# Kernel optimization log

Measured on AMD Instinct MI355X. Metric: run time of the kernel, lower is better.

The kernel has to match this reference:

```python
import jax, jax.numpy as jnp
import numpy as np
from jax import lax
import math

B, L, DQ, DK, DV = 4, 1024, 256, 256, 256
H, DE, DOUT, MAX_POS = 8, 64, 512, 32


def conv1d(x, w, b):
    # x: [b, c_in, l], w: [c_out, c_in, 3], pad=1 stride=1
    y = lax.conv_general_dilated(x, w, (1,), [(1, 1)],
                                 dimension_numbers=('NCH', 'OIH', 'NCH'))
    return y + b[None, :, None]


def aij(w_pos, n, max_pos):
    # relative-position table gather -> [q, k, d]
    idx = jnp.arange(n)
    rel = jnp.clip(idx[None, :] - idx[:, None], -max_pos, max_pos) + max_pos
    return w_pos[rel]


def setup_inputs() -> dict:
    key = jax.random.key(0)
    ks = jax.random.split(key, 12)
    s = 0.05
    return {
        'q': jax.random.normal(ks[0], (B, L, DQ), jnp.float32),
        'k': jax.random.normal(ks[1], (B, L, DK), jnp.float32),
        'v': jax.random.normal(ks[2], (B, L, DV), jnp.float32),
        'Wq': jax.random.normal(ks[3], (H * DE, DQ, 3), jnp.float32) * s,
        'bq': jnp.zeros((H * DE,), jnp.float32),
        'Wk': jax.random.normal(ks[4], (H * DE, DK, 3), jnp.float32) * s,
        'bk': jnp.zeros((H * DE,), jnp.float32),
        'Wv': jax.random.normal(ks[5], (DOUT, DV, 3), jnp.float32) * s,
        'bv': jnp.zeros((DOUT,), jnp.float32),
        'Wfc': jax.random.normal(ks[6], (DOUT, DOUT), jnp.float32) * s,
        'bfc': jnp.zeros((DOUT,), jnp.float32),
        'w_pos': jax.random.normal(ks[7], (2 * MAX_POS + 1, DE), jnp.float32),
        'attn_mask': jax.random.randint(ks[8], (1, 1, L, L), 0, 2) > 0,
        'valid_mask': jnp.zeros((1,), jnp.float32),
    }


def reference(q, k, v, Wq, bq, Wk, bk, Wv, bv, Wfc, bfc, w_pos, attn_mask, valid_mask):
    b, n_k = k.shape[0], k.shape[1]
    # b l c -> b c l, conv projections
    Q = conv1d(jnp.swapaxes(q, 1, 2), Wq, bq)   # [b, H*DE, l]
    K = conv1d(jnp.swapaxes(k, 1, 2), Wk, bk)
    V = conv1d(jnp.swapaxes(v, 1, 2), Wv, bv)   # [b, DOUT, l]
    # b (h d) l -> b h l d
    def split_heads(x, h):
        bb, hd, l = x.shape
        return jnp.transpose(x.reshape(bb, h, hd // h, l), (0, 1, 3, 2))
    Q_ = split_heads(Q, H)
    K_ = split_heads(K, H)
    V_ = split_heads(V, H)
    A = jnp.einsum('bhqd,bhkd->bhqk', Q_, K_) / math.sqrt(DE)
    A = A + jnp.einsum('bhqd,qkd->bhqk', Q_, aij(w_pos, n_k, MAX_POS))
    A = jnp.where(attn_mask, -jnp.inf, A)
    A = jax.nn.softmax(A, axis=-1)
    A = A * (A > valid_mask).astype(A.dtype)
    O = jnp.einsum('bhqk,bhkd->bhqd', A, V_)
    # b h n d -> b n (h d)
    O = jnp.transpose(O, (0, 2, 1, 3)).reshape(b, -1, DOUT)
    out = O @ Wfc.T + bfc
    return out, A
```

## Files before the change

### kernel.cpp

```cpp
#include <hip/hip_runtime.h>
#include <math.h>

typedef _Float16 f16;
typedef _Float16 f16x4 __attribute__((ext_vector_type(4)));
typedef _Float16 f16x8 __attribute__((ext_vector_type(8)));
typedef float f32x4 __attribute__((ext_vector_type(4)));

constexpr int B    = 4;
constexpr int L    = 1024;
constexpr int CIN  = 256;
constexpr int H    = 8;
constexpr int DOUT = 512;

__global__ void pack_kernel(const float* __restrict__ Wq, const float* __restrict__ Wk,
                            const float* __restrict__ Wv, f16* __restrict__ Wp)
{
    const int proj = blockIdx.y;
    const int co   = blockIdx.x;
    const int ci   = threadIdx.x;
    const float* W = (proj == 0) ? Wq : (proj == 1) ? Wk : Wv;
    f16* dst = Wp + ((size_t)proj * 512 + co) * 768;
    const float* src = W + (size_t)co * 768 + ci * 3;
    dst[0 * 256 + ci] = (f16)src[0];
    dst[1 * 256 + ci] = (f16)src[1];
    dst[2 * 256 + ci] = (f16)src[2];
}

__global__ __launch_bounds__(256) void convg_kernel(
    const float* __restrict__ qx, const float* __restrict__ kx, const float* __restrict__ vx,
    const f16* __restrict__ Wp,
    const float* __restrict__ bq, const float* __restrict__ bk, const float* __restrict__ bv,
    f16* __restrict__ Qh, f16* __restrict__ Kh, f16* __restrict__ Vt)
{
    const int proj = blockIdx.z;
    const float* __restrict__ x    = (proj == 0) ? qx : (proj == 1) ? kx : vx;
    const float* __restrict__ bias = (proj == 0) ? bq : (proj == 1) ? bk : bv;

    const int mt = blockIdx.x;
    const int b  = mt >> 3;
    const int l0 = (mt & 7) * 128;
    const int nb = blockIdx.y * 128;
    const int tid  = threadIdx.x;
    const int wvid = tid >> 6;
    const int lane = tid & 63;
    const int lg16 = lane & 15;
    const int lg4  = lane >> 4;
    const int wr = wvid >> 1, wc = wvid & 1;

    __shared__ __align__(16) f16 smem[3 * 128 * 72];
    f16* const Ah = smem;
    f16* const Al = smem + 128 * 72;
    f16* const Bs = smem + 2 * 128 * 72;
    f16* const Ct = smem;

    f32x4 acc[4][4];
#pragma unroll
    for (int mi = 0; mi < 4; ++mi)
#pragma unroll
        for (int ni = 0; ni < 4; ++ni) acc[mi][ni] = (f32x4){0.f, 0.f, 0.f, 0.f};

    const int r_st = tid >> 1;
    const int c_st = (tid & 1) * 32;

    for (int kc = 0; kc < 12; ++kc) {
        const int t = kc >> 2, ci0 = (kc & 3) << 6;
        __syncthreads();
        {
            const int l = l0 + r_st + t - 1;
            const bool ok = (l >= 0) && (l < L);
            const float* sx = x + ((size_t)b * L + (ok ? l : 0)) * CIN + ci0 + c_st;
#pragma unroll
            for (int g = 0; g < 4; ++g) {
                float4 v0 = make_float4(0.f, 0.f, 0.f, 0.f), v1 = v0;
                if (ok) { v0 = ((const float4*)sx)[g * 2]; v1 = ((const float4*)sx)[g * 2 + 1]; }
                float vv[8] = {v0.x, v0.y, v0.z, v0.w, v1.x, v1.y, v1.z, v1.w};
                f16 h8[8], l8[8];
#pragma unroll
                for (int i = 0; i < 8; ++i) {
                    h8[i] = (f16)vv[i];
                    l8[i] = (f16)(vv[i] - (float)h8[i]);
                }
                *(float4*)&Ah[r_st * 72 + c_st + g * 8] = *(const float4*)h8;
                *(float4*)&Al[r_st * 72 + c_st + g * 8] = *(const float4*)l8;
            }
        }
        {
            const f16* sw = Wp + ((size_t)proj * 512 + nb + r_st) * 768 + kc * 64 + c_st;
#pragma unroll
            for (int g = 0; g < 4; ++g)
                *(float4*)&Bs[r_st * 72 + c_st + g * 8] = ((const float4*)sw)[g];
        }
        __syncthreads();

#pragma unroll
        for (int ks = 0; ks < 2; ++ks) {
            f16x8 bb[4];
#pragma unroll
            for (int ni = 0; ni < 4; ++ni)
                bb[ni] = *(const f16x8*)&Bs[(wc * 64 + ni * 16 + lg16) * 72 + ks * 32 + lg4 * 8];
#pragma unroll
            for (int mi = 0; mi < 4; ++mi) {
                const f16x8 ah = *(const f16x8*)&Ah[(wr * 64 + mi * 16 + lg16) * 72 + ks * 32 + lg4 * 8];
                const f16x8 al = *(const f16x8*)&Al[(wr * 64 + mi * 16 + lg16) * 72 + ks * 32 + lg4 * 8];
#pragma unroll
                for (int ni = 0; ni < 4; ++ni) {
                    acc[mi][ni] = __builtin_amdgcn_mfma_f32_16x16x32_f16(ah, bb[ni], acc[mi][ni], 0, 0, 0);
                    acc[mi][ni] = __builtin_amdgcn_mfma_f32_16x16x32_f16(al, bb[ni], acc[mi][ni], 0, 0, 0);
                }
            }
        }
    }

    float bvv[4];
#pragma unroll
    for (int ni = 0; ni < 4; ++ni) bvv[ni] = bias[nb + wc * 64 + ni * 16 + lg16];
    __syncthreads();

    if (proj < 2) {
#pragma unroll
        for (int mi = 0; mi < 4; ++mi)
#pragma unroll
            for (int ni = 0; ni < 4; ++ni)
#pragma unroll
                for (int jr = 0; jr < 4; ++jr)
                    Ct[(wr * 64 + mi * 16 + lg4 * 4 + jr) * 136 + wc * 64 + ni * 16 + lg16] =
                        (f16)(acc[mi][ni][jr] + bvv[ni]);
        __syncthreads();
        f16* __restrict__ outp = (proj == 0) ? Qh : Kh;
        const int r = tid >> 1, hh = tid & 1;
        const int bh = b * 8 + (nb >> 6) + hh;
        float4* dst = (float4*)&outp[((size_t)bh * L + l0 + r) * 64];
        const float4* srcp = (const float4*)&Ct[r * 136 + hh * 64];
#pragma unroll
        for (int i = 0; i < 8; ++i) dst[i] = srcp[i];
    } else {
#pragma unroll
        for (int mi = 0; mi < 4; ++mi)
#pragma unroll
            for (int ni = 0; ni < 4; ++ni) {
                f16x4 pk = {(f16)(acc[mi][ni][0] + bvv[ni]), (f16)(acc[mi][ni][1] + bvv[ni]),
                            (f16)(acc[mi][ni][2] + bvv[ni]), (f16)(acc[mi][ni][3] + bvv[ni])};
                *(f16x4*)&Ct[(wc * 64 + ni * 16 + lg16) * 136 + wr * 64 + mi * 16 + lg4 * 4] = pk;
            }
        __syncthreads();
        const int r = tid >> 1, hh = tid & 1;
        float4* dst = (float4*)&Vt[((size_t)b * 512 + nb + r) * L + l0 + hh * 64];
        const float4* srcp = (const float4*)&Ct[r * 136 + hh * 64];
#pragma unroll
        for (int i = 0; i < 8; ++i) dst[i] = srcp[i];
    }
}

__global__ __launch_bounds__(256) void attn_kernel(
    const f16* __restrict__ Qh, const f16* __restrict__ Kh, const f16* __restrict__ Vt,
    const float* __restrict__ w_pos, const int* __restrict__ amask,
    const float* __restrict__ vmaskp,
    float* __restrict__ Aout, f16* __restrict__ Oh)
{
    const int bh = blockIdx.y;
    const int b = bh >> 3, h = bh & 7;
    const int q0 = blockIdx.x * 64;
    const int tid = threadIdx.x;
    const int wv   = tid >> 6;
    const int lane = tid & 63;
    const int lg16 = lane & 15;
    const int lg4  = lane >> 4;

    __shared__ __align__(16) f16  smem_h[4608 * 4];
    __shared__ __align__(16) float Ps[64 * 66];
    f16* const Qs = smem_h;
    f16* const Ks = smem_h + 4608;
    f16* const Vs = smem_h + 2 * 4608;
    f16* const es = smem_h + 3 * 4608;
    f16* const wps = Ks;

    float4 kreg[2], vreg[2];
#pragma unroll
    for (int p = 0; p < 2; ++p) {
        const int it = tid + p * 256, row = it >> 3, ch = it & 7;
        kreg[p] = *(const float4*)&Kh[((size_t)bh * L + row) * 64 + ch * 8];
        vreg[p] = *(const float4*)&Vt[((size_t)(bh * 64 + row)) * L + ch * 8];
    }

    for (int i = tid; i < 512; i += 256) {
        const int row = i >> 3, ch = i & 7;
        *(float4*)&Qs[row * 72 + ch * 8] =
            *(const float4*)&Qh[((size_t)bh * L + q0 + row) * 64 + ch * 8];
    }
    for (int i = tid; i < 640; i += 256) {
        const int r = i >> 3, ch = i & 7;
        f16 t[8];
        if (r < 65) {
            const float* s = w_pos + (size_t)r * 64 + ch * 8;
#pragma unroll
            for (int j = 0; j < 8; ++j) t[j] = (f16)s[j];
        } else {
#pragma unroll
            for (int j = 0; j < 8; ++j) t[j] = (f16)0.f;
        }
        *(float4*)&wps[r * 72 + ch * 8] = *(const float4*)t;
    }
    __syncthreads();

    f16x8 qa[2];
#pragma unroll
    for (int kc = 0; kc < 2; ++kc)
        qa[kc] = *(const f16x8*)&Qs[(wv * 16 + lg16) * 72 + kc * 32 + lg4 * 8];

#pragma unroll
    for (int c = 0; c < 5; ++c) {
        f32x4 acc = {0.f, 0.f, 0.f, 0.f};
#pragma unroll
        for (int kc = 0; kc < 2; ++kc) {
            f16x8 wb = *(const f16x8*)&wps[(c * 16 + lg16) * 72 + kc * 32 + lg4 * 8];
            acc = __builtin_amdgcn_mfma_f32_16x16x32_f16(qa[kc], wb, acc, 0, 0, 0);
        }
        const int r = c * 16 + lg16;
        if (r < 65) {
#pragma unroll
            for (int j = 0; j < 4; ++j)
                Ps[(wv * 16 + lg4 * 4 + j) * 66 + r] = acc[j];
        }
    }

    float mrow[4], lrow[4];
#pragma unroll
    for (int j = 0; j < 4; ++j) { mrow[j] = -INFINITY; lrow[j] = 0.f; }
    f32x4 Oc[4];
#pragma unroll
    for (int c = 0; c < 4; ++c) Oc[c] = (f32x4){0.f, 0.f, 0.f, 0.f};

    const int qloc0 = wv * 16 + lg4 * 4;
    const size_t Abase = ((size_t)bh * L + q0 + qloc0) * L;

    for (int kt = 0; kt < 16; ++kt) {
        const int kbase = kt * 64;
        __syncthreads();
#pragma unroll
        for (int p = 0; p < 2; ++p) {
            const int it = tid + p * 256, row = it >> 3, ch = it & 7;
            *(float4*)&Ks[row * 72 + ch * 8] = kreg[p];
            *(float4*)&Vs[row * 72 + ch * 8] = vreg[p];
        }
        __syncthreads();
        if (kt < 15) {
            const int kb2 = kbase + 64;
#pragma unroll
            for (int p = 0; p < 2; ++p) {
                const int it = tid + p * 256, row = it >> 3, ch = it & 7;
                kreg[p] = *(const float4*)&Kh[((size_t)bh * L + kb2 + row) * 64 + ch * 8];
                vreg[p] = *(const float4*)&Vt[((size_t)(bh * 64 + row)) * L + kb2 + ch * 8];
            }
        }

        f32x4 sc[4];
#pragma unroll
        for (int c = 0; c < 4; ++c) {
            sc[c] = (f32x4){0.f, 0.f, 0.f, 0.f};
#pragma unroll
            for (int kc = 0; kc < 2; ++kc) {
                f16x8 kb = *(const f16x8*)&Ks[(c * 16 + lg16) * 72 + kc * 32 + lg4 * 8];
                sc[c] = __builtin_amdgcn_mfma_f32_16x16x32_f16(qa[kc], kb, sc[c], 0, 0, 0);
            }
        }

        float sv[4][4];
#pragma unroll
        for (int c = 0; c < 4; ++c) {
            const int kg = kbase + c * 16 + lg16;
#pragma unroll
            for (int j = 0; j < 4; ++j) {
                const int ql = qloc0 + j;
                const int qg = q0 + ql;
                int off = kg - qg;
                off = off < -32 ? -32 : (off > 32 ? 32 : off);
                float v = sc[c][j] * 0.125f + Ps[ql * 66 + off + 32];
                if (amask[(size_t)qg * L + kg] != 0) v = -INFINITY;
                Aout[Abase + (size_t)j * L + kg] = v;
                sv[c][j] = v;
            }
        }

        float mn[4], al[4];
#pragma unroll
        for (int j = 0; j < 4; ++j) {
            float t = fmaxf(fmaxf(sv[0][j], sv[1][j]), fmaxf(sv[2][j], sv[3][j]));
            t = fmaxf(t, __shfl_xor(t, 1, 64));
            t = fmaxf(t, __shfl_xor(t, 2, 64));
            t = fmaxf(t, __shfl_xor(t, 4, 64));
            t = fmaxf(t, __shfl_xor(t, 8, 64));
            mn[j] = fmaxf(mrow[j], t);
        }
#pragma unroll
        for (int j = 0; j < 4; ++j) {
            float s = 0.f;
            if (mn[j] == -INFINITY) {
                al[j] = 1.f;
#pragma unroll
                for (int c = 0; c < 4; ++c) sv[c][j] = 0.f;
            } else {
                al[j] = __expf(mrow[j] - mn[j]);
#pragma unroll
                for (int c = 0; c < 4; ++c) { sv[c][j] = __expf(sv[c][j] - mn[j]); s += sv[c][j]; }
            }
            s += __shfl_xor(s, 1, 64);
            s += __shfl_xor(s, 2, 64);
            s += __shfl_xor(s, 4, 64);
            s += __shfl_xor(s, 8, 64);
            lrow[j] = lrow[j] * al[j] + s;
            mrow[j] = mn[j];
        }

#pragma unroll
        for (int c = 0; c < 4; ++c)
#pragma unroll
            for (int j = 0; j < 4; ++j)
                es[(qloc0 + j) * 72 + c * 16 + lg16] = (f16)sv[c][j];
        asm volatile("s_waitcnt lgkmcnt(0)" ::: "memory");
        __builtin_amdgcn_sched_barrier(0);
#pragma unroll
        for (int c = 0; c < 4; ++c)
#pragma unroll
            for (int j = 0; j < 4; ++j)
                Oc[c][j] *= al[j];

        f16x8 ea[2];
#pragma unroll
        for (int kc = 0; kc < 2; ++kc)
            ea[kc] = *(const f16x8*)&es[(wv * 16 + lg16) * 72 + kc * 32 + lg4 * 8];
#pragma unroll
        for (int c = 0; c < 4; ++c)
#pragma unroll
            for (int kc = 0; kc < 2; ++kc) {
                f16x8 vb = *(const f16x8*)&Vs[(c * 16 + lg16) * 72 + kc * 32 + lg4 * 8];
                Oc[c] = __builtin_amdgcn_mfma_f32_16x16x32_f16(ea[kc], vb, Oc[c], 0, 0, 0);
            }
    }

    float il[4];
#pragma unroll
    for (int j = 0; j < 4; ++j) il[j] = lrow[j] > 0.f ? 1.f / lrow[j] : 0.f;
#pragma unroll
    for (int c = 0; c < 4; ++c)
#pragma unroll
        for (int j = 0; j < 4; ++j)
            Oh[((size_t)b * L + q0 + qloc0 + j) * DOUT + h * 64 + c * 16 + lg16] =
                (f16)(Oc[c][j] * il[j]);

    const float vm = vmaskp[0];
    for (int kt = 0; kt < 16; ++kt) {
#pragma unroll
        for (int c = 0; c < 4; ++c) {
            const int kg = kt * 64 + c * 16 + lg16;
#pragma unroll
            for (int j = 0; j < 4; ++j) {
                const size_t ad = Abase + (size_t)j * L + kg;
                const float s = Aout[ad];
                float a = (mrow[j] == -INFINITY) ? 0.f : __expf(s - mrow[j]) * il[j];
                if (!(a > vm)) a = 0.f;
                Aout[ad] = a;
            }
        }
    }
}

__global__ __launch_bounds__(256) void fcg_kernel(
    const f16* __restrict__ Ohp, const float* __restrict__ Wfc,
    const float* __restrict__ bfc, float* __restrict__ outp)
{
    const int Mb = blockIdx.x * 128;
    const int Nb = blockIdx.y * 128;
    const int tid  = threadIdx.x;
    const int wvid = tid >> 6;
    const int lane = tid & 63;
    const int lg16 = lane & 15;
    const int lg4  = lane >> 4;
    const int wr = wvid >> 1, wc = wvid & 1;

    __shared__ __align__(16) f16 As[128 * 72];
    __shared__ __align__(16) f16 Bs[128 * 72];

    f32x4 acc[4][4];
#pragma unroll
    for (int mi = 0; mi < 4; ++mi)
#pragma unroll
        for (int ni = 0; ni < 4; ++ni) acc[mi][ni] = (f32x4){0.f, 0.f, 0.f, 0.f};

    const int r_st = tid >> 1;
    const int c_st = (tid & 1) * 32;

    for (int kc = 0; kc < 8; ++kc) {
        __syncthreads();
        {
            const f16* s = Ohp + (size_t)(Mb + r_st) * DOUT + kc * 64 + c_st;
#pragma unroll
            for (int g = 0; g < 4; ++g)
                *(float4*)&As[r_st * 72 + c_st + g * 8] = ((const float4*)s)[g];
        }
        {
            const float* s = Wfc + (size_t)(Nb + r_st) * DOUT + kc * 64 + c_st;
#pragma unroll
            for (int g = 0; g < 4; ++g) {
                float4 v0 = ((const float4*)s)[g * 2];
                float4 v1 = ((const float4*)s)[g * 2 + 1];
                f16 t[8] = {(f16)v0.x, (f16)v0.y, (f16)v0.z, (f16)v0.w,
                            (f16)v1.x, (f16)v1.y, (f16)v1.z, (f16)v1.w};
                *(float4*)&Bs[r_st * 72 + c_st + g * 8] = *(const float4*)t;
            }
        }
        __syncthreads();

#pragma unroll
        for (int ks = 0; ks < 2; ++ks) {
            f16x8 bb[4];
#pragma unroll
            for (int ni = 0; ni < 4; ++ni)
                bb[ni] = *(const f16x8*)&Bs[(wc * 64 + ni * 16 + lg16) * 72 + ks * 32 + lg4 * 8];
#pragma unroll
            for (int mi = 0; mi < 4; ++mi) {
                const f16x8 aa = *(const f16x8*)&As[(wr * 64 + mi * 16 + lg16) * 72 + ks * 32 + lg4 * 8];
#pragma unroll
                for (int ni = 0; ni < 4; ++ni)
                    acc[mi][ni] = __builtin_amdgcn_mfma_f32_16x16x32_f16(aa, bb[ni], acc[mi][ni], 0, 0, 0);
            }
        }
    }

#pragma unroll
    for (int ni = 0; ni < 4; ++ni) {
        const int col = Nb + wc * 64 + ni * 16 + lg16;
        const float bv = bfc[col];
#pragma unroll
        for (int mi = 0; mi < 4; ++mi) {
            const int row0 = Mb + wr * 64 + mi * 16 + lg4 * 4;
#pragma unroll
            for (int jr = 0; jr < 4; ++jr)
                outp[(size_t)(row0 + jr) * DOUT + col] = acc[mi][ni][jr] + bv;
        }
    }
}

extern "C" void kernel_launch(void* const* d_in, const int* in_sizes, int n_in,
                              void* d_out, int out_size, void* d_ws, size_t ws_size,
                              hipStream_t stream) {
    const float* q    = (const float*)d_in[0];
    const float* k    = (const float*)d_in[1];
    const float* v    = (const float*)d_in[2];
    const float* Wq   = (const float*)d_in[3];
    const float* bq   = (const float*)d_in[4];
    const float* Wk   = (const float*)d_in[5];
    const float* bk   = (const float*)d_in[6];
    const float* Wv   = (const float*)d_in[7];
    const float* bv   = (const float*)d_in[8];
    const float* Wfc  = (const float*)d_in[9];
    const float* bfc  = (const float*)d_in[10];
    const float* wpos = (const float*)d_in[11];
    const int*   amsk = (const int*)d_in[12];
    const float* vmsk = (const float*)d_in[13];

    f16* Qh  = (f16*)d_ws;
    f16* Kh  = Qh  + (size_t)2097152;
    f16* Vt  = Kh  + (size_t)2097152;
    f16* Ohh = Vt  + (size_t)2097152;
    f16* Wp  = Ohh + (size_t)2097152;

    float* outp = (float*)d_out;
    float* Aout = outp + (size_t)B * L * DOUT;

    pack_kernel<<<dim3(512, 3), 256, 0, stream>>>(Wq, Wk, Wv, Wp);
    convg_kernel<<<dim3(32, 4, 3), 256, 0, stream>>>(
        q, k, v, Wp, bq, bk, bv, Qh, Kh, Vt);
    attn_kernel<<<dim3(L / 64, B * H), 256, 0, stream>>>(
        Qh, Kh, Vt, wpos, amsk, vmsk, Aout, Ohh);
    fcg_kernel<<<dim3(32, 4), 256, 0, stream>>>(
        Ohh, Wfc, bfc, outp);
}
```

Before: 432.8 us.

## Use two-pass softmax to avoid storing and rereading raw attention scores

The attention kernel becomes two passes. The first pass computes QK^T plus the positional bias only to get the row max and sum, and records the masked positions as per-thread bit masks. The second pass recomputes the scores, writes the final normalized and thresholded probabilities to Aout once, and uses the same values for the PV matmul, so the output rescale step goes away. This removes the write-then-read-then-write round trip of the large Aout tensor and the second amask read, at the cost of doing the QK MFMAs twice and loading K twice.

```diff
diff --git a/kernel.cpp b/kernel.cpp
--- a/kernel.cpp
+++ b/kernel.cpp
@@ -174,14 +174,6 @@
     f16* const es = smem_h + 3 * 4608;
     f16* const wps = Ks;
 
-    float4 kreg[2], vreg[2];
-#pragma unroll
-    for (int p = 0; p < 2; ++p) {
-        const int it = tid + p * 256, row = it >> 3, ch = it & 7;
-        kreg[p] = *(const float4*)&Kh[((size_t)bh * L + row) * 64 + ch * 8];
-        vreg[p] = *(const float4*)&Vt[((size_t)(bh * 64 + row)) * L + ch * 8];
-    }
-
     for (int i = tid; i < 512; i += 256) {
         const int row = i >> 3, ch = i & 7;
         *(float4*)&Qs[row * 72 + ch * 8] =
@@ -223,15 +215,20 @@
         }
     }
 
-    float mrow[4], lrow[4];
-#pragma unroll
-    for (int j = 0; j < 4; ++j) { mrow[j] = -INFINITY; lrow[j] = 0.f; }
-    f32x4 Oc[4];
-#pragma unroll
-    for (int c = 0; c < 4; ++c) Oc[c] = (f32x4){0.f, 0.f, 0.f, 0.f};
-
     const int qloc0 = wv * 16 + lg4 * 4;
     const size_t Abase = ((size_t)bh * L + q0 + qloc0) * L;
+
+    float mrow[4], lrow[4];
+#pragma unroll
+    for (int j = 0; j < 4; ++j) { mrow[j] = -INFINITY; lrow[j] = 0.f; }
+    unsigned int mbits[8] = {0, 0, 0, 0, 0, 0, 0, 0};
+
+    float4 kreg[2];
+#pragma unroll
+    for (int p = 0; p < 2; ++p) {
+        const int it = tid + p * 256, row = it >> 3, ch = it & 7;
+        kreg[p] = *(const float4*)&Kh[((size_t)bh * L + row) * 64 + ch * 8];
+    }
 
     for (int kt = 0; kt < 16; ++kt) {
         const int kbase = kt * 64;
@@ -240,7 +237,6 @@
         for (int p = 0; p < 2; ++p) {
             const int it = tid + p * 256, row = it >> 3, ch = it & 7;
             *(float4*)&Ks[row * 72 + ch * 8] = kreg[p];
-            *(float4*)&Vs[row * 72 + ch * 8] = vreg[p];
         }
         __syncthreads();
         if (kt < 15) {
@@ -249,7 +245,6 @@
             for (int p = 0; p < 2; ++p) {
                 const int it = tid + p * 256, row = it >> 3, ch = it & 7;
                 kreg[p] = *(const float4*)&Kh[((size_t)bh * L + kb2 + row) * 64 + ch * 8];
-                vreg[p] = *(const float4*)&Vt[((size_t)(bh * 64 + row)) * L + kb2 + ch * 8];
             }
         }
 
@@ -275,13 +270,15 @@
                 int off = kg - qg;
                 off = off < -32 ? -32 : (off > 32 ? 32 : off);
                 float v = sc[c][j] * 0.125f + Ps[ql * 66 + off + 32];
-                if (amask[(size_t)qg * L + kg] != 0) v = -INFINITY;
-                Aout[Abase + (size_t)j * L + kg] = v;
+                if (amask[(size_t)qg * L + kg] != 0) {
+                    v = -INFINITY;
+                    mbits[kt >> 1] |= 1u << ((kt & 1) * 16 + c * 4 + j);
+                }
                 sv[c][j] = v;
             }
         }
 
-        float mn[4], al[4];
+        float mn[4];
 #pragma unroll
         for (int j = 0; j < 4; ++j) {
             float t = fmaxf(fmaxf(sv[0][j], sv[1][j]), fmaxf(sv[2][j], sv[3][j]));
@@ -293,36 +290,95 @@
         }
 #pragma unroll
         for (int j = 0; j < 4; ++j) {
-            float s = 0.f;
+            float s = 0.f, al;
             if (mn[j] == -INFINITY) {
-                al[j] = 1.f;
-#pragma unroll
-                for (int c = 0; c < 4; ++c) sv[c][j] = 0.f;
+                al = 1.f;
             } else {
-                al[j] = __expf(mrow[j] - mn[j]);
-#pragma unroll
-                for (int c = 0; c < 4; ++c) { sv[c][j] = __expf(sv[c][j] - mn[j]); s += sv[c][j]; }
+                al = __expf(mrow[j] - mn[j]);
+#pragma unroll
+                for (int c = 0; c < 4; ++c) s += __expf(sv[c][j] - mn[j]);
             }
             s += __shfl_xor(s, 1, 64);
             s += __shfl_xor(s, 2, 64);
             s += __shfl_xor(s, 4, 64);
             s += __shfl_xor(s, 8, 64);
-            lrow[j] = lrow[j] * al[j] + s;
+            lrow[j] = lrow[j] * al + s;
             mrow[j] = mn[j];
         }
-
-#pragma unroll
-        for (int c = 0; c < 4; ++c)
-#pragma unroll
-            for (int j = 0; j < 4; ++j)
-                es[(qloc0 + j) * 72 + c * 16 + lg16] = (f16)sv[c][j];
+    }
+
+    float il[4];
+#pragma unroll
+    for (int j = 0; j < 4; ++j) il[j] = lrow[j] > 0.f ? 1.f / lrow[j] : 0.f;
+    const float vm = vmaskp[0];
+
+    f32x4 Oc[4];
+#pragma unroll
+    for (int c = 0; c < 4; ++c) Oc[c] = (f32x4){0.f, 0.f, 0.f, 0.f};
+
+    float4 vreg[2];
+#pragma unroll
+    for (int p = 0; p < 2; ++p) {
+        const int it = tid + p * 256, row = it >> 3, ch = it & 7;
+        kreg[p] = *(const float4*)&Kh[((size_t)bh * L + row) * 64 + ch * 8];
+        vreg[p] = *(const float4*)&Vt[((size_t)(bh * 64 + row)) * L + ch * 8];
+    }
+
+    for (int kt = 0; kt < 16; ++kt) {
+        const int kbase = kt * 64;
+        __syncthreads();
+#pragma unroll
+        for (int p = 0; p < 2; ++p) {
+            const int it = tid + p * 256, row = it >> 3, ch = it & 7;
+            *(float4*)&Ks[row * 72 + ch * 8] = kreg[p];
+            *(float4*)&Vs[row * 72 + ch * 8] = vreg[p];
+        }
+        __syncthreads();
+        if (kt < 15) {
+            const int kb2 = kbase + 64;
+#pragma unroll
+            for (int p = 0; p < 2; ++p) {
+                const int it = tid + p * 256, row = it >> 3, ch = it & 7;
+                kreg[p] = *(const float4*)&Kh[((size_t)bh * L + kb2 + row) * 64 + ch * 8];
+                vreg[p] = *(const float4*)&Vt[((size_t)(bh * 64 + row)) * L + kb2 + ch * 8];
+            }
+        }
+
+        f32x4 sc[4];
+#pragma unroll
+        for (int c = 0; c < 4; ++c) {
+            sc[c] = (f32x4){0.f, 0.f, 0.f, 0.f};
+#pragma unroll
+            for (int kc = 0; kc < 2; ++kc) {
+                f16x8 kb = *(const f16x8*)&Ks[(c * 16 + lg16) * 72 + kc * 32 + lg4 * 8];
+                sc[c] = __builtin_amdgcn_mfma_f32_16x16x32_f16(qa[kc], kb, sc[c], 0, 0, 0);
+            }
+        }
+
+        const unsigned int mw = mbits[kt >> 1] >> ((kt & 1) * 16);
+#pragma unroll
+        for (int c = 0; c < 4; ++c) {
+            const int kg = kbase + c * 16 + lg16;
+#pragma unroll
+            for (int j = 0; j < 4; ++j) {
+                const int ql = qloc0 + j;
+                const int qg = q0 + ql;
+                float a;
+                if (((mw >> (c * 4 + j)) & 1u) || mrow[j] == -INFINITY) {
+                    a = 0.f;
+                } else {
+                    int off = kg - qg;
+                    off = off < -32 ? -32 : (off > 32 ? 32 : off);
+                    const float s = sc[c][j] * 0.125f + Ps[ql * 66 + off + 32];
+                    a = __expf(s - mrow[j]) * il[j];
+                }
+                if (!(a > vm)) a = 0.f;
+                Aout[Abase + (size_t)j * L + kg] = a;
+                es[(ql) * 72 + c * 16 + lg16] = (f16)a;
+            }
+        }
         asm volatile("s_waitcnt lgkmcnt(0)" ::: "memory");
         __builtin_amdgcn_sched_barrier(0);
-#pragma unroll
-        for (int c = 0; c < 4; ++c)
-#pragma unroll
-            for (int j = 0; j < 4; ++j)
-                Oc[c][j] *= al[j];
 
         f16x8 ea[2];
 #pragma unroll
@@ -337,31 +393,12 @@
             }
     }
 
-    float il[4];
-#pragma unroll
-    for (int j = 0; j < 4; ++j) il[j] = lrow[j] > 0.f ? 1.f / lrow[j] : 0.f;
 #pragma unroll
     for (int c = 0; c < 4; ++c)
 #pragma unroll
         for (int j = 0; j < 4; ++j)
             Oh[((size_t)b * L + q0 + qloc0 + j) * DOUT + h * 64 + c * 16 + lg16] =
-                (f16)(Oc[c][j] * il[j]);
-
-    const float vm = vmaskp[0];
-    for (int kt = 0; kt < 16; ++kt) {
-#pragma unroll
-        for (int c = 0; c < 4; ++c) {
-            const int kg = kt * 64 + c * 16 + lg16;
-#pragma unroll
-            for (int j = 0; j < 4; ++j) {
-                const size_t ad = Abase + (size_t)j * L + kg;
-                const float s = Aout[ad];
-                float a = (mrow[j] == -INFINITY) ? 0.f : __expf(s - mrow[j]) * il[j];
-                if (!(a > vm)) a = 0.f;
-                Aout[ad] = a;
-            }
-        }
-    }
+                (f16)Oc[c][j];
 }
 
 __global__ __launch_bounds__(256) void fcg_kernel(
```

After: 388.5 us. 10.2% less time.
